# Kernel optimization log

Measured on AMD Instinct MI355X. Metric: run time of the kernel, lower is better.

## Reference

```python
import jax, jax.numpy as jnp
from jax import lax
import numpy as np

B, N_MEL, T_MEL = 256, 80, 800
R = 16                      # n_frames_per_step
RNN = 1024                  # decoder_rnn_dim
ENC = 256                   # token_embedding_size
MEL_DIM = N_MEL * R         # 1280, == RNN + ENC (LSTMCell input size)
IN_DIM = RNN + ENC          # 1280


def setup_inputs() -> dict:
    key = jax.random.key(0)
    ks = jax.random.split(key, 10)
    s = 0.02
    return {
        "context": jax.random.normal(ks[0], (B, ENC), dtype=jnp.float32),
        "target": jax.random.normal(ks[1], (B, N_MEL, T_MEL), dtype=jnp.float32),
        "W_ih": jax.random.normal(ks[2], (4 * RNN, IN_DIM), dtype=jnp.float32) * s,
        "b_ih": jnp.zeros((4 * RNN,), dtype=jnp.float32),
        "W_hh": jax.random.normal(ks[3], (4 * RNN, RNN), dtype=jnp.float32) * s,
        "b_hh": jnp.zeros((4 * RNN,), dtype=jnp.float32),
        "W_proj": jax.random.normal(ks[4], (MEL_DIM, IN_DIM), dtype=jnp.float32) * s,
        "b_proj": jnp.zeros((MEL_DIM,), dtype=jnp.float32),
        "W_gate": jax.random.normal(ks[5], (1, IN_DIM), dtype=jnp.float32) * s,
        "b_gate": jnp.zeros((1,), dtype=jnp.float32),
    }


def _decoder_forward(context, target, W_ih, b_ih, W_hh, b_hh, W_proj, b_proj, W_gate, b_gate):
    b = context.shape[0]
    n_mel, t_mel = target.shape[1], target.shape[2]
    mel_dim = W_proj.shape[0]
    r = mel_dim // n_mel                      # n_frames_per_step
    T = t_mel // r                            # decoder steps
    rnn = W_hh.shape[1]

    # parse_decoder_inputs: [B, n_mel, T_mel] -> [T, B, mel_dim]
    frames = target.transpose(0, 2, 1).reshape(b, T, mel_dim).transpose(1, 0, 2)
    # step 0 uses the all-zeros go frame; step t>=1 uses target frame t (teacher forcing, p=1)
    inputs = frames.at[0].set(0.0)

    h0 = jnp.zeros((b, rnn), dtype=context.dtype)
    c0 = jnp.zeros((b, rnn), dtype=context.dtype)

    def step(carry, x):
        h, c = carry
        gates = x @ W_ih.T + b_ih + h @ W_hh.T + b_hh   # [B, 4*rnn]
        i, f, g, o = jnp.split(gates, 4, axis=-1)        # torch LSTMCell gate order
        c_new = jax.nn.sigmoid(f) * c + jax.nn.sigmoid(i) * jnp.tanh(g)
        h_new = jax.nn.sigmoid(o) * jnp.tanh(c_new)
        # eval mode: dropout on c is identity
        oc = jnp.concatenate([h_new, context], axis=1)   # [B, rnn+enc]
        mel = oc @ W_proj.T + b_proj                     # [B, mel_dim]
        gate = oc @ W_gate.T + b_gate                    # [B, 1]
        return (h_new, c_new), (mel, gate)

    _, (mels, gates) = lax.scan(step, (h0, c0), inputs)
    # mels: [T, B, mel_dim] -> [B, n_mel, T_mel]
    mel_outputs = mels.transpose(1, 0, 2).reshape(b, T * r, n_mel).transpose(0, 2, 1)
    gate_outputs = gates.transpose(1, 0, 2)              # [B, T, 1]
    return mel_outputs, gate_outputs


def reference(context, target, W_ih, b_ih, W_hh, b_hh, W_proj, b_proj, W_gate, b_gate):
    return _decoder_forward(context, target, W_ih, b_ih, W_hh, b_hh,
                            W_proj, b_proj, W_gate, b_gate)
```

## Files before the change

### kernel.cpp

```cpp
#include <hip/hip_runtime.h>
#include <hip/hip_bf16.h>
#include <math.h>

#define BB     256
#define NMEL   80
#define TMEL   800
#define NFR    16
#define TT     50
#define RNN    1024
#define ENC    256
#define INDIM  1280
#define G4     4096
#define MROWS  (TT*BB)

typedef __attribute__((ext_vector_type(8))) short bf16x8;
typedef __attribute__((ext_vector_type(4))) float f32x4;

#define GAS __attribute__((address_space(1)))
#define LAS __attribute__((address_space(3)))

__device__ __forceinline__ unsigned short f2bf(float f) {
    unsigned int u = __float_as_uint(f);
    u += 0x7FFFu + ((u >> 16) & 1u);
    return (unsigned short)(u >> 16);
}
__device__ __forceinline__ float bf2f(unsigned short s) {
    return __uint_as_float(((unsigned int)s) << 16);
}
__device__ __forceinline__ float fsig(float x) {
    return 1.f / (1.f + __expf(-x));
}
__device__ __forceinline__ float ftanh(float x) {
    return 2.f / (1.f + __expf(-2.f * x)) - 1.f;
}


__global__ void k_f32_to_bf16(const float* __restrict__ src,
                              unsigned short* __restrict__ dst, int n4) {
    for (int i = blockIdx.x * blockDim.x + threadIdx.x; i < n4;
         i += gridDim.x * blockDim.x) {
        f32x4 v = *(const f32x4*)(src + (size_t)i * 4);
        unsigned long long p = (unsigned long long)f2bf(v[0]) |
                               ((unsigned long long)f2bf(v[1]) << 16) |
                               ((unsigned long long)f2bf(v[2]) << 32) |
                               ((unsigned long long)f2bf(v[3]) << 48);
        *(unsigned long long*)(dst + (size_t)i * 4) = p;
    }
}

__global__ void k_conv_wph(const float* __restrict__ wproj,
                           unsigned short* __restrict__ dst) {
    const int n4 = INDIM * RNN / 4;
    for (int i = blockIdx.x * blockDim.x + threadIdx.x; i < n4;
         i += gridDim.x * blockDim.x) {
        int mp = i >> 8, kc = (i & 255) * 4;
        int mel = mp >> 4, fr = mp & 15;
        f32x4 v = *(const f32x4*)(wproj + (size_t)(fr * NMEL + mel) * INDIM + kc);
        unsigned long long p = (unsigned long long)f2bf(v[0]) |
                               ((unsigned long long)f2bf(v[1]) << 16) |
                               ((unsigned long long)f2bf(v[2]) << 32) |
                               ((unsigned long long)f2bf(v[3]) << 48);
        *(unsigned long long*)(dst + (size_t)i * 4) = p;
    }
}

__global__ void k_conv_wpc(const float* __restrict__ wproj,
                           unsigned short* __restrict__ dst) {
    const int n4 = INDIM * ENC / 4;
    for (int i = blockIdx.x * blockDim.x + threadIdx.x; i < n4;
         i += gridDim.x * blockDim.x) {
        int mp = i >> 6, kc = (i & 63) * 4;
        int mel = mp >> 4, fr = mp & 15;
        f32x4 v = *(const f32x4*)(wproj + (size_t)(fr * NMEL + mel) * INDIM +
                                  RNN + kc);
        unsigned long long p = (unsigned long long)f2bf(v[0]) |
                               ((unsigned long long)f2bf(v[1]) << 16) |
                               ((unsigned long long)f2bf(v[2]) << 32) |
                               ((unsigned long long)f2bf(v[3]) << 48);
        *(unsigned long long*)(dst + (size_t)i * 4) = p;
    }
}

__global__ __launch_bounds__(128) void k_frames(const float* __restrict__ target,
                                                unsigned short* __restrict__ frames) {
    const int wg = blockIdx.x;
    const int t = wg >> 8, b = wg & 255;
    unsigned short* dst = frames + ((size_t)t * BB + b) * INDIM;
    if (t == 0) {
        for (int i = threadIdx.x; i < INDIM / 8; i += 128)
            *(f32x4*)(dst + i * 8) = (f32x4){0.f, 0.f, 0.f, 0.f};
        return;
    }
    __shared__ float ld[NMEL][17];
    for (int i = threadIdx.x; i < 320; i += 128) {
        const int mel = i >> 2, fq = i & 3;
        f32x4 v = *(const f32x4*)(target + ((size_t)b * NMEL + mel) * TMEL +
                                  t * NFR + fq * 4);
        #pragma unroll
        for (int j = 0; j < 4; ++j) ld[mel][fq * 4 + j] = v[j];
    }
    __syncthreads();
    for (int i = threadIdx.x; i < 160; i += 128) {
        unsigned long long p0 = 0, p1 = 0;
        #pragma unroll
        for (int j = 0; j < 4; ++j) {
            const int k = i * 8 + j;
            p0 |= (unsigned long long)f2bf(ld[k % 80][k / 80]) << (16 * j);
        }
        #pragma unroll
        for (int j = 0; j < 4; ++j) {
            const int k = i * 8 + 4 + j;
            p1 |= (unsigned long long)f2bf(ld[k % 80][k / 80]) << (16 * j);
        }
        *(unsigned long long*)(dst + i * 8) = p0;
        *(unsigned long long*)(dst + i * 8 + 4) = p1;
    }
}

__global__ void k_gatectx(const float* __restrict__ context,
                          const float* __restrict__ wgate,
                          const float* __restrict__ bgate,
                          float* __restrict__ gctx) {
    int b = blockIdx.x * blockDim.x + threadIdx.x;
    if (b >= BB) return;
    float acc = bgate[0];
    const float* cb = context + b * ENC;
    for (int e = 0; e < ENC; ++e) acc += cb[e] * wgate[RNN + e];
    gctx[b] = acc;
}

template<int STRIDE, int KDIM>
__device__ __forceinline__ void gemm_core3(const unsigned short* __restrict__ A,
                                           const unsigned short* __restrict__ Bw,
                                           int mblk, int nblk,
                                           unsigned short* As,
                                           unsigned short* Bs,
                                           f32x4 acc[4][2]) {
    const int tid = threadIdx.x, lane = tid & 63, w = tid >> 6;
    const int lr = lane & 15, q = lane >> 4;
    const int wm = (w >> 2) * 64, wn = (w & 3) * 32;
    const int cc1 = tid, cc2 = tid + 512;
    const int r1 = cc1 >> 3, s1 = ((cc1 & 7) ^ (r1 & 7)) * 8;
    const int r2 = cc2 >> 3, s2 = ((cc2 & 7) ^ (r2 & 7)) * 8;
    const unsigned short* a1p = A + (size_t)(mblk + r1) * STRIDE + s1;
    const unsigned short* a2p = A + (size_t)(mblk + r2) * STRIDE + s2;
    const unsigned short* b1p = Bw + (size_t)(nblk + r1) * STRIDE + s1;
    const unsigned short* b2p = Bw + (size_t)(nblk + r2) * STRIDE + s2;

#define GSTAGE(buf, k0) do {                                                   \
    __builtin_amdgcn_global_load_lds((const GAS unsigned int*)(a1p + (k0)),    \
        (LAS unsigned int*)(As + (buf) * 8192 + w * 512), 16, 0, 0);           \
    __builtin_amdgcn_global_load_lds((const GAS unsigned int*)(a2p + (k0)),    \
        (LAS unsigned int*)(As + (buf) * 8192 + 4096 + w * 512), 16, 0, 0);    \
    __builtin_amdgcn_global_load_lds((const GAS unsigned int*)(b1p + (k0)),    \
        (LAS unsigned int*)(Bs + (buf) * 8192 + w * 512), 16, 0, 0);           \
    __builtin_amdgcn_global_load_lds((const GAS unsigned int*)(b2p + (k0)),    \
        (LAS unsigned int*)(Bs + (buf) * 8192 + 4096 + w * 512), 16, 0, 0); } while (0)

    constexpr int NIT = KDIM / 64;
    GSTAGE(0, 0); GSTAGE(1, 64);
    #pragma unroll 3
    for (int it = 0; it < NIT; ++it) {
        if (it < NIT - 1) asm volatile("s_waitcnt vmcnt(4)" ::: "memory");
        else              asm volatile("s_waitcnt vmcnt(0)" ::: "memory");
        asm volatile("s_waitcnt lgkmcnt(0)" ::: "memory");
        asm volatile("s_barrier" ::: "memory");
        __builtin_amdgcn_sched_barrier(0);
        if (it <= NIT - 3) GSTAGE((it + 2) % 3, (it + 2) * 64);
        const unsigned short* Ab = As + (it % 3) * 8192;
        const unsigned short* Bb = Bs + (it % 3) * 8192;
        #pragma unroll
        for (int ks = 0; ks < 2; ++ks) {
            const int j = (((ks * 4 + q) ^ (lr & 7)) * 8);
            bf16x8 af[4], bv[2];
            #pragma unroll
            for (int mi = 0; mi < 4; ++mi)
                af[mi] = *(const bf16x8*)(Ab + (wm + mi * 16 + lr) * 64 + j);
            #pragma unroll
            for (int ni = 0; ni < 2; ++ni)
                bv[ni] = *(const bf16x8*)(Bb + (wn + ni * 16 + lr) * 64 + j);
            #pragma unroll
            for (int mi = 0; mi < 4; ++mi)
                #pragma unroll
                for (int ni = 0; ni < 2; ++ni)
                    acc[mi][ni] = __builtin_amdgcn_mfma_f32_16x16x32_bf16(
                        af[mi], bv[ni], acc[mi][ni], 0, 0, 0);
        }
    }
#undef GSTAGE
}

__global__ __launch_bounds__(512) void k_gemm_xproj(
    const unsigned short* __restrict__ A,
    const unsigned short* __restrict__ Bw,
    const float* __restrict__ b_ih, const float* __restrict__ b_hh,
    unsigned short* __restrict__ Cout)
{
    __shared__ unsigned short As[3][8192], Bs[3][8192];
    f32x4 acc[4][2] = {};
    const int mblk = blockIdx.y * 128, nblk = blockIdx.x * 128;
    gemm_core3<INDIM, INDIM>(A, Bw, mblk, nblk, &As[0][0], &Bs[0][0], acc);
    const int lane = threadIdx.x & 63, w = threadIdx.x >> 6;
    const int wm = (w >> 2) * 64, wn = (w & 3) * 32;
    const int lr = lane & 15, q = lane >> 4;
    #pragma unroll
    for (int ni = 0; ni < 2; ++ni) {
        const int col = nblk + wn + ni * 16 + lr;
        const float bias = b_ih[col] + b_hh[col];
        #pragma unroll
        for (int mi = 0; mi < 4; ++mi) {
            const int row0 = mblk + wm + mi * 16 + q * 4;
            #pragma unroll
            for (int r = 0; r < 4; ++r)
                Cout[(size_t)(row0 + r) * G4 + col] = f2bf(acc[mi][ni][r] + bias);
        }
    }
}

__global__ __launch_bounds__(512) void k_gemm_mel(
    const unsigned short* __restrict__ A,
    const unsigned short* __restrict__ Bw,
    const float* __restrict__ ctxproj,
    float* __restrict__ out0)
{
    __shared__ unsigned short As[3][8192], Bs[3][8192];
    __shared__ float txp[8][16][20];
    f32x4 acc[4][2] = {};
    const int mblk = blockIdx.y * 128, nblk = blockIdx.x * 128;
    gemm_core3<RNN, RNN>(A, Bw, mblk, nblk, &As[0][0], &Bs[0][0], acc);
    const int lane = threadIdx.x & 63, w = threadIdx.x >> 6;
    const int wm = (w >> 2) * 64, wn = (w & 3) * 32;
    const int lr = lane & 15, q = lane >> 4;
    const int rbase = q * 4;
    const int rowl = lane & 15, fq = lane >> 4;
    #pragma unroll
    for (int mi = 0; mi < 4; ++mi) {
        const int row0 = mblk + wm + mi * 16;
        const int t = row0 >> 8, b0 = row0 & 255;
        #pragma unroll
        for (int ni = 0; ni < 2; ++ni) {
            const int colbase = nblk + wn + ni * 16;
            const int mel = colbase >> 4;
            #pragma unroll
            for (int r = 0; r < 4; ++r)
                txp[w][rbase + r][lr] = acc[mi][ni][r];
            const int bL = b0 + rowl;
            f32x4 v = *(const f32x4*)&txp[w][rowl][fq * 4];
            f32x4 cx = *(const f32x4*)(ctxproj + (size_t)bL * INDIM +
                                       mel * 16 + fq * 4);
            *(f32x4*)(out0 + (size_t)(bL * NMEL + mel) * TMEL +
                      t * NFR + fq * 4) = v + cx;
        }
    }
}

__global__ __launch_bounds__(512) void k_gemm_ctx(
    const unsigned short* __restrict__ A,
    const unsigned short* __restrict__ Bw,
    const float* __restrict__ bproj,
    float* __restrict__ ctxout)
{
    __shared__ unsigned short As[3][8192], Bs[3][8192];
    f32x4 acc[4][2] = {};
    const int mblk = blockIdx.y * 128, nblk = blockIdx.x * 128;
    gemm_core3<ENC, ENC>(A, Bw, mblk, nblk, &As[0][0], &Bs[0][0], acc);
    const int lane = threadIdx.x & 63, w = threadIdx.x >> 6;
    const int wm = (w >> 2) * 64, wn = (w & 3) * 32;
    const int lr = lane & 15, q = lane >> 4;
    #pragma unroll
    for (int ni = 0; ni < 2; ++ni) {
        const int mp = nblk + wn + ni * 16 + lr;
        const int mel = mp >> 4, fr = mp & 15;
        const float bias = bproj[fr * NMEL + mel];
        #pragma unroll
        for (int mi = 0; mi < 4; ++mi) {
            const int b0 = mblk + wm + mi * 16 + q * 4;
            #pragma unroll
            for (int r = 0; r < 4; ++r)
                ctxout[(size_t)(b0 + r) * INDIM + mp] = acc[mi][ni][r] + bias;
        }
    }
}

__global__ __launch_bounds__(512) void k_step(
    const unsigned short* __restrict__ Whh,
    const unsigned short* __restrict__ xproj_t,
    const unsigned short* __restrict__ h_prev,
    unsigned short* __restrict__ h_next,
    float* __restrict__ c)
{
    __shared__ unsigned short Abuf[3][8192];
    __shared__ unsigned short Bbuf[3][8192];
    __shared__ unsigned short xg[4096];
    __shared__ float cld[64][16];
    __shared__ float gates[4][64][17];
    const int tid = threadIdx.x, lane = tid & 63, w = tid >> 6;
    const int g = w & 3, mh = w >> 2;
    const int n0 = blockIdx.x * 16, m0 = blockIdx.y * 64;
    const int lr = lane & 15, q = lane >> 4;

    const int cc1 = tid, cc2 = tid + 512;
    const int r1 = cc1 >> 4, s1g = (cc1 & 15) ^ (r1 & 15);
    const int r2 = cc2 >> 4, s2g = (cc2 & 15) ^ (r2 & 15);
    const unsigned short* a1src = h_prev + (size_t)(m0 + r1) * RNN + s1g * 8;
    const unsigned short* a2src = h_prev + (size_t)(m0 + r2) * RNN + s2g * 8;
    const unsigned short* b1src = Whh +
        (size_t)((r1 >> 4) * RNN + n0 + (r1 & 15)) * RNN + s1g * 8;
    const unsigned short* b2src = Whh +
        (size_t)((r2 >> 4) * RNN + n0 + (r2 & 15)) * RNN + s2g * 8;
    const unsigned short* xsrc = xproj_t +
        (size_t)(m0 + ((tid >> 1) & 63)) * G4 + (tid >> 7) * RNN + n0 +
        (tid & 1) * 8;
    const float* csrc = c + (size_t)(m0 + (tid >> 2)) * RNN + n0 + (tid & 3) * 4;

#define STAGE(buf, k0) do {                                                    \
    __builtin_amdgcn_global_load_lds((const GAS unsigned int*)(a1src + (k0)),  \
        (LAS unsigned int*)&Abuf[buf][w * 512], 16, 0, 0);                     \
    __builtin_amdgcn_global_load_lds((const GAS unsigned int*)(a2src + (k0)),  \
        (LAS unsigned int*)&Abuf[buf][4096 + w * 512], 16, 0, 0);              \
    __builtin_amdgcn_global_load_lds((const GAS unsigned int*)(b1src + (k0)),  \
        (LAS unsigned int*)&Bbuf[buf][w * 512], 16, 0, 0);                     \
    __builtin_amdgcn_global_load_lds((const GAS unsigned int*)(b2src + (k0)),  \
        (LAS unsigned int*)&Bbuf[buf][4096 + w * 512], 16, 0, 0); } while (0)

    if (w < 4)
        __builtin_amdgcn_global_load_lds((const GAS unsigned int*)csrc,
            (LAS unsigned int*)&cld[w * 16][0], 16, 0, 0);
    __builtin_amdgcn_global_load_lds((const GAS unsigned int*)xsrc,
        (LAS unsigned int*)&xg[w * 512], 16, 0, 0);
    STAGE(0, 0); STAGE(1, 128);

    f32x4 acc[2] = {};
    #pragma unroll
    for (int it = 0; it < 8; ++it) {
        if (it <= 6) asm volatile("s_waitcnt vmcnt(4)" ::: "memory");
        else         asm volatile("s_waitcnt vmcnt(0)" ::: "memory");
        asm volatile("s_waitcnt lgkmcnt(0)" ::: "memory");
        asm volatile("s_barrier" ::: "memory");
        __builtin_amdgcn_sched_barrier(0);
        if (it <= 5) STAGE((it + 2) % 3, (it + 2) * 128);
        const unsigned short* Ab = Abuf[it % 3];
        const unsigned short* Bb = Bbuf[it % 3];
        #pragma unroll
        for (int ks = 0; ks < 4; ++ks) {
            const int j = ((ks * 4 + q) ^ lr) * 8;
            bf16x8 a0 = *(const bf16x8*)(Ab + (mh * 32 + lr) * 128 + j);
            bf16x8 a1 = *(const bf16x8*)(Ab + (mh * 32 + 16 + lr) * 128 + j);
            bf16x8 bv = *(const bf16x8*)(Bb + (g * 16 + lr) * 128 + j);
            acc[0] = __builtin_amdgcn_mfma_f32_16x16x32_bf16(a0, bv, acc[0], 0, 0, 0);
            acc[1] = __builtin_amdgcn_mfma_f32_16x16x32_bf16(a1, bv, acc[1], 0, 0, 0);
        }
    }

    #pragma unroll
    for (int mi = 0; mi < 2; ++mi)
        #pragma unroll
        for (int r = 0; r < 4; ++r) {
            const int row = mh * 32 + mi * 16 + q * 4 + r;
            gates[g][row][lr] = acc[mi][r] +
                bf2f(xg[(g * 64 + row) * 16 + lr]);
        }
    __syncthreads();

    #pragma unroll
    for (int q2 = 0; q2 < 2; ++q2) {
        const int e = tid + q2 * 512;
        const int row = e >> 4, col = e & 15;
        const int b = m0 + row, j = n0 + col;
        const float xi = gates[0][row][col];
        const float xf = gates[1][row][col];
        const float xgt = gates[2][row][col];
        const float xo = gates[3][row][col];
        const float si = fsig(xi);
        const float sf = fsig(xf);
        const float so = fsig(xo);
        const float cp = cld[row][col];
        const float cn = sf * cp + si * ftanh(xgt);
        const float hn = so * ftanh(cn);
        c[(size_t)b * RNN + j] = cn;
        h_next[(size_t)b * RNN + j] = f2bf(hn);
    }
#undef STAGE
}

__global__ void k_gate(const unsigned short* __restrict__ h,
                       const float* __restrict__ wgate,
                       const float* __restrict__ gctx,
                       float* __restrict__ out1) {
    const int gw = (blockIdx.x * blockDim.x + threadIdx.x) >> 6;
    const int lane = threadIdx.x & 63;
    if (gw >= MROWS) return;
    const unsigned short* hr = h + (size_t)gw * RNN + lane * 16;
    const float* wr = wgate + lane * 16;
    float acc = 0.f;
    #pragma unroll
    for (int j = 0; j < 16; ++j) acc += bf2f(hr[j]) * wr[j];
    for (int off = 32; off; off >>= 1) acc += __shfl_down(acc, off);
    if (lane == 0) {
        const int t = gw >> 8, b = gw & 255;
        out1[b * TT + t] = acc + gctx[b];
    }
}

static const size_t OFF_WIH   = 0;
static const size_t OFF_WHH   = OFF_WIH   + (size_t)G4 * INDIM * 2;
static const size_t OFF_WPH   = OFF_WHH   + (size_t)G4 * RNN * 2;
static const size_t OFF_WPC   = OFF_WPH   + (size_t)INDIM * RNN * 2;
static const size_t OFF_CTXB  = OFF_WPC   + (size_t)INDIM * ENC * 2;
static const size_t OFF_FRM   = OFF_CTXB  + (size_t)BB * ENC * 2;
static const size_t OFF_XPROJ = OFF_FRM   + (size_t)MROWS * INDIM * 2;
static const size_t OFF_HALL  = OFF_XPROJ + (size_t)MROWS * G4 * 2;
static const size_t OFF_C     = OFF_HALL  + (size_t)(TT + 1) * BB * RNN * 2;
static const size_t OFF_CTX   = OFF_C     + (size_t)BB * RNN * 4;
static const size_t OFF_GCTX  = OFF_CTX   + (size_t)BB * INDIM * 4;

extern "C" void kernel_launch(void* const* d_in, const int* in_sizes, int n_in,
                              void* d_out, int out_size, void* d_ws, size_t ws_size,
                              hipStream_t stream) {
    const float* context = (const float*)d_in[0];
    const float* target  = (const float*)d_in[1];
    const float* W_ih    = (const float*)d_in[2];
    const float* b_ih    = (const float*)d_in[3];
    const float* W_hh    = (const float*)d_in[4];
    const float* b_hh    = (const float*)d_in[5];
    const float* W_proj  = (const float*)d_in[6];
    const float* b_proj  = (const float*)d_in[7];
    const float* W_gate  = (const float*)d_in[8];
    const float* b_gate  = (const float*)d_in[9];
    float* out = (float*)d_out;
    char* ws = (char*)d_ws;

    unsigned short* wih_bf  = (unsigned short*)(ws + OFF_WIH);
    unsigned short* whh_bf  = (unsigned short*)(ws + OFF_WHH);
    unsigned short* wph_bf  = (unsigned short*)(ws + OFF_WPH);
    unsigned short* wpc_bf  = (unsigned short*)(ws + OFF_WPC);
    unsigned short* ctx_bf  = (unsigned short*)(ws + OFF_CTXB);
    unsigned short* frames  = (unsigned short*)(ws + OFF_FRM);
    unsigned short* xproj   = (unsigned short*)(ws + OFF_XPROJ);
    unsigned short* h_all   = (unsigned short*)(ws + OFF_HALL);
    float*          c_buf   = (float*)(ws + OFF_C);
    float*          ctxproj = (float*)(ws + OFF_CTX);
    float*          gctx    = (float*)(ws + OFF_GCTX);

    hipMemsetAsync(h_all, 0, (size_t)BB * RNN * 2, stream);
    hipMemsetAsync(c_buf, 0, (size_t)BB * RNN * 4, stream);

    k_f32_to_bf16<<<2048, 256, 0, stream>>>(W_ih, wih_bf, G4 * INDIM / 4);
    k_f32_to_bf16<<<2048, 256, 0, stream>>>(W_hh, whh_bf, G4 * RNN / 4);
    k_conv_wph<<<2048, 256, 0, stream>>>(W_proj, wph_bf);
    k_conv_wpc<<<320, 256, 0, stream>>>(W_proj, wpc_bf);
    k_f32_to_bf16<<<64, 256, 0, stream>>>(context, ctx_bf, BB * ENC / 4);
    k_frames<<<MROWS, 128, 0, stream>>>(target, frames);
    k_gatectx<<<1, 256, 0, stream>>>(context, W_gate, b_gate, gctx);

    k_gemm_ctx<<<dim3(INDIM / 128, BB / 128), 512, 0, stream>>>(
        ctx_bf, wpc_bf, b_proj, ctxproj);

    k_gemm_xproj<<<dim3(G4 / 128, MROWS / 128), 512, 0, stream>>>(
        frames, wih_bf, b_ih, b_hh, xproj);

    for (int t = 0; t < TT; ++t) {
        k_step<<<dim3(64, 4), 512, 0, stream>>>(
            whh_bf, xproj + (size_t)t * BB * G4,
            h_all + (size_t)t * BB * RNN,
            h_all + (size_t)(t + 1) * BB * RNN, c_buf);
    }

    k_gemm_mel<<<dim3(INDIM / 128, MROWS / 128), 512, 0, stream>>>(
        h_all + (size_t)BB * RNN, wph_bf, ctxproj, out);
    k_gate<<<MROWS / 4, 256, 0, stream>>>(h_all + (size_t)BB * RNN, W_gate,
                                          gctx, out + (size_t)BB * NMEL * TMEL);
}
```

Measured before the change: 729.7 us.

## Use double-buffered GEMM pipeline and smaller K-tiles in recurrent step kernel

The shared GEMM core changes from a triple-buffered, two-ahead prefetch to a double-buffered scheme. It issues the next stage before waiting and adds a trailing barrier after compute. This lowers LDS usage per block, which may raise occupancy, but costs an extra barrier per K iteration. The per-step LSTM recurrent kernel now uses 64-wide K tiles with 16 iterations instead of 128-wide with 8, halving its LDS staging buffers. In exchange it runs more loop iterations and barriers inside the latency-critical sequential step.

```diff
diff --git a/kernel.cpp b/kernel.cpp
--- a/kernel.cpp
+++ b/kernel.cpp
@@ -130,7 +130,7 @@
 }
 
 template<int STRIDE, int KDIM>
-__device__ __forceinline__ void gemm_core3(const unsigned short* __restrict__ A,
+__device__ __forceinline__ void gemm_core2(const unsigned short* __restrict__ A,
                                            const unsigned short* __restrict__ Bw,
                                            int mblk, int nblk,
                                            unsigned short* As,
@@ -158,17 +158,19 @@
         (LAS unsigned int*)(Bs + (buf) * 8192 + 4096 + w * 512), 16, 0, 0); } while (0)
 
     constexpr int NIT = KDIM / 64;
-    GSTAGE(0, 0); GSTAGE(1, 64);
-    #pragma unroll 3
+    GSTAGE(0, 0);
+    #pragma unroll 4
     for (int it = 0; it < NIT; ++it) {
-        if (it < NIT - 1) asm volatile("s_waitcnt vmcnt(4)" ::: "memory");
-        else              asm volatile("s_waitcnt vmcnt(0)" ::: "memory");
-        asm volatile("s_waitcnt lgkmcnt(0)" ::: "memory");
+        if (it < NIT - 1) {
+            GSTAGE((it + 1) & 1, (it + 1) * 64);
+            asm volatile("s_waitcnt vmcnt(4)" ::: "memory");
+        } else {
+            asm volatile("s_waitcnt vmcnt(0)" ::: "memory");
+        }
         asm volatile("s_barrier" ::: "memory");
         __builtin_amdgcn_sched_barrier(0);
-        if (it <= NIT - 3) GSTAGE((it + 2) % 3, (it + 2) * 64);
-        const unsigned short* Ab = As + (it % 3) * 8192;
-        const unsigned short* Bb = Bs + (it % 3) * 8192;
+        const unsigned short* Ab = As + (it & 1) * 8192;
+        const unsigned short* Bb = Bs + (it & 1) * 8192;
         #pragma unroll
         for (int ks = 0; ks < 2; ++ks) {
             const int j = (((ks * 4 + q) ^ (lr & 7)) * 8);
@@ -186,6 +188,9 @@
                     acc[mi][ni] = __builtin_amdgcn_mfma_f32_16x16x32_bf16(
                         af[mi], bv[ni], acc[mi][ni], 0, 0, 0);
         }
+        asm volatile("s_waitcnt lgkmcnt(0)" ::: "memory");
+        __builtin_amdgcn_sched_barrier(0);
+        asm volatile("s_barrier" ::: "memory");
     }
 #undef GSTAGE
 }
@@ -196,10 +201,10 @@
     const float* __restrict__ b_ih, const float* __restrict__ b_hh,
     unsigned short* __restrict__ Cout)
 {
-    __shared__ unsigned short As[3][8192], Bs[3][8192];
+    __shared__ unsigned short As[2][8192], Bs[2][8192];
     f32x4 acc[4][2] = {};
     const int mblk = blockIdx.y * 128, nblk = blockIdx.x * 128;
-    gemm_core3<INDIM, INDIM>(A, Bw, mblk, nblk, &As[0][0], &Bs[0][0], acc);
+    gemm_core2<INDIM, INDIM>(A, Bw, mblk, nblk, &As[0][0], &Bs[0][0], acc);
     const int lane = threadIdx.x & 63, w = threadIdx.x >> 6;
     const int wm = (w >> 2) * 64, wn = (w & 3) * 32;
     const int lr = lane & 15, q = lane >> 4;
@@ -223,11 +228,11 @@
     const float* __restrict__ ctxproj,
     float* __restrict__ out0)
 {
-    __shared__ unsigned short As[3][8192], Bs[3][8192];
+    __shared__ unsigned short As[2][8192], Bs[2][8192];
     __shared__ float txp[8][16][20];
     f32x4 acc[4][2] = {};
     const int mblk = blockIdx.y * 128, nblk = blockIdx.x * 128;
-    gemm_core3<RNN, RNN>(A, Bw, mblk, nblk, &As[0][0], &Bs[0][0], acc);
+    gemm_core2<RNN, RNN>(A, Bw, mblk, nblk, &As[0][0], &Bs[0][0], acc);
     const int lane = threadIdx.x & 63, w = threadIdx.x >> 6;
     const int wm = (w >> 2) * 64, wn = (w & 3) * 32;
     const int lr = lane & 15, q = lane >> 4;
@@ -260,10 +265,10 @@
     const float* __restrict__ bproj,
     float* __restrict__ ctxout)
 {
-    __shared__ unsigned short As[3][8192], Bs[3][8192];
+    __shared__ unsigned short As[2][8192], Bs[2][8192];
     f32x4 acc[4][2] = {};
     const int mblk = blockIdx.y * 128, nblk = blockIdx.x * 128;
-    gemm_core3<ENC, ENC>(A, Bw, mblk, nblk, &As[0][0], &Bs[0][0], acc);
+    gemm_core2<ENC, ENC>(A, Bw, mblk, nblk, &As[0][0], &Bs[0][0], acc);
     const int lane = threadIdx.x & 63, w = threadIdx.x >> 6;
     const int wm = (w >> 2) * 64, wn = (w & 3) * 32;
     const int lr = lane & 15, q = lane >> 4;
@@ -289,8 +294,8 @@
     unsigned short* __restrict__ h_next,
     float* __restrict__ c)
 {
-    __shared__ unsigned short Abuf[3][8192];
-    __shared__ unsigned short Bbuf[3][8192];
+    __shared__ unsigned short Abuf[3][4096];
+    __shared__ unsigned short Bbuf[3][4096];
     __shared__ unsigned short xg[4096];
     __shared__ float cld[64][16];
     __shared__ float gates[4][64][17];
@@ -299,54 +304,46 @@
     const int n0 = blockIdx.x * 16, m0 = blockIdx.y * 64;
     const int lr = lane & 15, q = lane >> 4;
 
-    const int cc1 = tid, cc2 = tid + 512;
-    const int r1 = cc1 >> 4, s1g = (cc1 & 15) ^ (r1 & 15);
-    const int r2 = cc2 >> 4, s2g = (cc2 & 15) ^ (r2 & 15);
-    const unsigned short* a1src = h_prev + (size_t)(m0 + r1) * RNN + s1g * 8;
-    const unsigned short* a2src = h_prev + (size_t)(m0 + r2) * RNN + s2g * 8;
-    const unsigned short* b1src = Whh +
-        (size_t)((r1 >> 4) * RNN + n0 + (r1 & 15)) * RNN + s1g * 8;
-    const unsigned short* b2src = Whh +
-        (size_t)((r2 >> 4) * RNN + n0 + (r2 & 15)) * RNN + s2g * 8;
+    const int rowc = tid >> 3, sc = ((tid & 7) ^ (rowc & 7)) * 8;
+    const unsigned short* asrc = h_prev + (size_t)(m0 + rowc) * RNN + sc;
+    const unsigned short* bsrc = Whh +
+        (size_t)((rowc >> 4) * RNN + n0 + (rowc & 15)) * RNN + sc;
     const unsigned short* xsrc = xproj_t +
         (size_t)(m0 + ((tid >> 1) & 63)) * G4 + (tid >> 7) * RNN + n0 +
         (tid & 1) * 8;
     const float* csrc = c + (size_t)(m0 + (tid >> 2)) * RNN + n0 + (tid & 3) * 4;
 
 #define STAGE(buf, k0) do {                                                    \
-    __builtin_amdgcn_global_load_lds((const GAS unsigned int*)(a1src + (k0)),  \
+    __builtin_amdgcn_global_load_lds((const GAS unsigned int*)(asrc + (k0)),   \
         (LAS unsigned int*)&Abuf[buf][w * 512], 16, 0, 0);                     \
-    __builtin_amdgcn_global_load_lds((const GAS unsigned int*)(a2src + (k0)),  \
-        (LAS unsigned int*)&Abuf[buf][4096 + w * 512], 16, 0, 0);              \
-    __builtin_amdgcn_global_load_lds((const GAS unsigned int*)(b1src + (k0)),  \
-        (LAS unsigned int*)&Bbuf[buf][w * 512], 16, 0, 0);                     \
-    __builtin_amdgcn_global_load_lds((const GAS unsigned int*)(b2src + (k0)),  \
-        (LAS unsigned int*)&Bbuf[buf][4096 + w * 512], 16, 0, 0); } while (0)
+    __builtin_amdgcn_global_load_lds((const GAS unsigned int*)(bsrc + (k0)),   \
+        (LAS unsigned int*)&Bbuf[buf][w * 512], 16, 0, 0); } while (0)
 
     if (w < 4)
         __builtin_amdgcn_global_load_lds((const GAS unsigned int*)csrc,
             (LAS unsigned int*)&cld[w * 16][0], 16, 0, 0);
     __builtin_amdgcn_global_load_lds((const GAS unsigned int*)xsrc,
         (LAS unsigned int*)&xg[w * 512], 16, 0, 0);
-    STAGE(0, 0); STAGE(1, 128);
+    STAGE(0, 0); STAGE(1, 64); STAGE(2, 128);
 
     f32x4 acc[2] = {};
     #pragma unroll
-    for (int it = 0; it < 8; ++it) {
-        if (it <= 6) asm volatile("s_waitcnt vmcnt(4)" ::: "memory");
-        else         asm volatile("s_waitcnt vmcnt(0)" ::: "memory");
+    for (int it = 0; it < 16; ++it) {
+        if (it <= 13)      asm volatile("s_waitcnt vmcnt(4)" ::: "memory");
+        else if (it == 14) asm volatile("s_waitcnt vmcnt(2)" ::: "memory");
+        else               asm volatile("s_waitcnt vmcnt(0)" ::: "memory");
         asm volatile("s_waitcnt lgkmcnt(0)" ::: "memory");
         asm volatile("s_barrier" ::: "memory");
         __builtin_amdgcn_sched_barrier(0);
-        if (it <= 5) STAGE((it + 2) % 3, (it + 2) * 128);
+        if (it <= 13) STAGE((it + 2) % 3, (it + 2) * 64);
         const unsigned short* Ab = Abuf[it % 3];
         const unsigned short* Bb = Bbuf[it % 3];
         #pragma unroll
-        for (int ks = 0; ks < 4; ++ks) {
-            const int j = ((ks * 4 + q) ^ lr) * 8;
-            bf16x8 a0 = *(const bf16x8*)(Ab + (mh * 32 + lr) * 128 + j);
-            bf16x8 a1 = *(const bf16x8*)(Ab + (mh * 32 + 16 + lr) * 128 + j);
-            bf16x8 bv = *(const bf16x8*)(Bb + (g * 16 + lr) * 128 + j);
+        for (int ks = 0; ks < 2; ++ks) {
+            const int j = (((ks * 4 + q) ^ (lr & 7)) * 8);
+            bf16x8 a0 = *(const bf16x8*)(Ab + (mh * 32 + lr) * 64 + j);
+            bf16x8 a1 = *(const bf16x8*)(Ab + (mh * 32 + 16 + lr) * 64 + j);
+            bf16x8 bv = *(const bf16x8*)(Bb + (g * 16 + lr) * 64 + j);
             acc[0] = __builtin_amdgcn_mfma_f32_16x16x32_bf16(a0, bv, acc[0], 0, 0, 0);
             acc[1] = __builtin_amdgcn_mfma_f32_16x16x32_bf16(a1, bv, acc[1], 0, 0, 0);
         }
```

New measurement: 801.5 us. 1.1x slower.

## Restructure batched GEMMs to 4 waves with 64x64 warp tiles and fragment-major LDS

Applied to the files above, without the earlier changes.

The shared GEMM core moves from 8 waves with 64x32 warp tiles and a BK=64 XOR-swizzled LDS stage to 4 waves with 64x64 warp tiles and a BK=32 stage. The stage is stored in MFMA fragment order, so each lane reads its 16-byte operand at lane*8 with no swizzle. The aim is more MFMA work per LDS fragment load and a smaller LDS footprint, which could allow more blocks per CU. The cost is twice as many k-iterations and barriers per tile, and more accumulator registers per thread. Only the pre- and post-recurrence GEMMs change; the 50 sequential step kernels are untouched.

```diff
diff --git a/kernel.cpp b/kernel.cpp
--- a/kernel.cpp
+++ b/kernel.cpp
@@ -130,81 +130,76 @@
 }
 
 template<int STRIDE, int KDIM>
-__device__ __forceinline__ void gemm_core3(const unsigned short* __restrict__ A,
+__device__ __forceinline__ void gemm_core4(const unsigned short* __restrict__ A,
                                            const unsigned short* __restrict__ Bw,
                                            int mblk, int nblk,
                                            unsigned short* As,
                                            unsigned short* Bs,
-                                           f32x4 acc[4][2]) {
+                                           f32x4 acc[4][4]) {
     const int tid = threadIdx.x, lane = tid & 63, w = tid >> 6;
-    const int lr = lane & 15, q = lane >> 4;
-    const int wm = (w >> 2) * 64, wn = (w & 3) * 32;
-    const int cc1 = tid, cc2 = tid + 512;
-    const int r1 = cc1 >> 3, s1 = ((cc1 & 7) ^ (r1 & 7)) * 8;
-    const int r2 = cc2 >> 3, s2 = ((cc2 & 7) ^ (r2 & 7)) * 8;
-    const unsigned short* a1p = A + (size_t)(mblk + r1) * STRIDE + s1;
-    const unsigned short* a2p = A + (size_t)(mblk + r2) * STRIDE + s2;
-    const unsigned short* b1p = Bw + (size_t)(nblk + r1) * STRIDE + s1;
-    const unsigned short* b2p = Bw + (size_t)(nblk + r2) * STRIDE + s2;
+    const int wm = (w >> 1) * 64, wn = (w & 1) * 64;
+    const int c1 = tid, c2 = tid + 256;
+    const int r1 = (c1 >> 6) * 16 + (c1 & 15), k1 = ((c1 >> 4) & 3) * 8;
+    const int r2 = (c2 >> 6) * 16 + (c2 & 15), k2 = ((c2 >> 4) & 3) * 8;
+    const unsigned short* a1p = A + (size_t)(mblk + r1) * STRIDE + k1;
+    const unsigned short* a2p = A + (size_t)(mblk + r2) * STRIDE + k2;
+    const unsigned short* b1p = Bw + (size_t)(nblk + r1) * STRIDE + k1;
+    const unsigned short* b2p = Bw + (size_t)(nblk + r2) * STRIDE + k2;
 
 #define GSTAGE(buf, k0) do {                                                   \
     __builtin_amdgcn_global_load_lds((const GAS unsigned int*)(a1p + (k0)),    \
-        (LAS unsigned int*)(As + (buf) * 8192 + w * 512), 16, 0, 0);           \
+        (LAS unsigned int*)(As + (buf) * 4096 + w * 512), 16, 0, 0);           \
     __builtin_amdgcn_global_load_lds((const GAS unsigned int*)(a2p + (k0)),    \
-        (LAS unsigned int*)(As + (buf) * 8192 + 4096 + w * 512), 16, 0, 0);    \
+        (LAS unsigned int*)(As + (buf) * 4096 + 2048 + w * 512), 16, 0, 0);    \
     __builtin_amdgcn_global_load_lds((const GAS unsigned int*)(b1p + (k0)),    \
-        (LAS unsigned int*)(Bs + (buf) * 8192 + w * 512), 16, 0, 0);           \
+        (LAS unsigned int*)(Bs + (buf) * 4096 + w * 512), 16, 0, 0);           \
     __builtin_amdgcn_global_load_lds((const GAS unsigned int*)(b2p + (k0)),    \
-        (LAS unsigned int*)(Bs + (buf) * 8192 + 4096 + w * 512), 16, 0, 0); } while (0)
-
-    constexpr int NIT = KDIM / 64;
-    GSTAGE(0, 0); GSTAGE(1, 64);
-    #pragma unroll 3
+        (LAS unsigned int*)(Bs + (buf) * 4096 + 2048 + w * 512), 16, 0, 0); } while (0)
+
+    constexpr int NIT = KDIM / 32;
+    GSTAGE(0, 0); GSTAGE(1, 32);
+    #pragma unroll 4
     for (int it = 0; it < NIT; ++it) {
         if (it < NIT - 1) asm volatile("s_waitcnt vmcnt(4)" ::: "memory");
         else              asm volatile("s_waitcnt vmcnt(0)" ::: "memory");
         asm volatile("s_waitcnt lgkmcnt(0)" ::: "memory");
         asm volatile("s_barrier" ::: "memory");
         __builtin_amdgcn_sched_barrier(0);
-        if (it <= NIT - 3) GSTAGE((it + 2) % 3, (it + 2) * 64);
-        const unsigned short* Ab = As + (it % 3) * 8192;
-        const unsigned short* Bb = Bs + (it % 3) * 8192;
-        #pragma unroll
-        for (int ks = 0; ks < 2; ++ks) {
-            const int j = (((ks * 4 + q) ^ (lr & 7)) * 8);
-            bf16x8 af[4], bv[2];
+        if (it <= NIT - 3) GSTAGE((it + 2) % 3, (it + 2) * 32);
+        const unsigned short* Ab = As + (it % 3) * 4096;
+        const unsigned short* Bb = Bs + (it % 3) * 4096;
+        bf16x8 af[4], bv[4];
+        #pragma unroll
+        for (int mi = 0; mi < 4; ++mi)
+            af[mi] = *(const bf16x8*)(Ab + ((wm >> 4) + mi) * 512 + lane * 8);
+        #pragma unroll
+        for (int ni = 0; ni < 4; ++ni)
+            bv[ni] = *(const bf16x8*)(Bb + ((wn >> 4) + ni) * 512 + lane * 8);
+        #pragma unroll
+        for (int mi = 0; mi < 4; ++mi)
             #pragma unroll
-            for (int mi = 0; mi < 4; ++mi)
-                af[mi] = *(const bf16x8*)(Ab + (wm + mi * 16 + lr) * 64 + j);
-            #pragma unroll
-            for (int ni = 0; ni < 2; ++ni)
-                bv[ni] = *(const bf16x8*)(Bb + (wn + ni * 16 + lr) * 64 + j);
-            #pragma unroll
-            for (int mi = 0; mi < 4; ++mi)
-                #pragma unroll
-                for (int ni = 0; ni < 2; ++ni)
-                    acc[mi][ni] = __builtin_amdgcn_mfma_f32_16x16x32_bf16(
-                        af[mi], bv[ni], acc[mi][ni], 0, 0, 0);
-        }
+            for (int ni = 0; ni < 4; ++ni)
+                acc[mi][ni] = __builtin_amdgcn_mfma_f32_16x16x32_bf16(
+                    af[mi], bv[ni], acc[mi][ni], 0, 0, 0);
     }
 #undef GSTAGE
 }
 
-__global__ __launch_bounds__(512) void k_gemm_xproj(
+__global__ __launch_bounds__(256) void k_gemm_xproj(
     const unsigned short* __restrict__ A,
     const unsigned short* __restrict__ Bw,
     const float* __restrict__ b_ih, const float* __restrict__ b_hh,
     unsigned short* __restrict__ Cout)
 {
-    __shared__ unsigned short As[3][8192], Bs[3][8192];
-    f32x4 acc[4][2] = {};
+    __shared__ unsigned short As[3][4096], Bs[3][4096];
+    f32x4 acc[4][4] = {};
     const int mblk = blockIdx.y * 128, nblk = blockIdx.x * 128;
-    gemm_core3<INDIM, INDIM>(A, Bw, mblk, nblk, &As[0][0], &Bs[0][0], acc);
+    gemm_core4<INDIM, INDIM>(A, Bw, mblk, nblk, &As[0][0], &Bs[0][0], acc);
     const int lane = threadIdx.x & 63, w = threadIdx.x >> 6;
-    const int wm = (w >> 2) * 64, wn = (w & 3) * 32;
+    const int wm = (w >> 1) * 64, wn = (w & 1) * 64;
     const int lr = lane & 15, q = lane >> 4;
     #pragma unroll
-    for (int ni = 0; ni < 2; ++ni) {
+    for (int ni = 0; ni < 4; ++ni) {
         const int col = nblk + wn + ni * 16 + lr;
         const float bias = b_ih[col] + b_hh[col];
         #pragma unroll
@@ -217,19 +212,19 @@
     }
 }
 
-__global__ __launch_bounds__(512) void k_gemm_mel(
+__global__ __launch_bounds__(256) void k_gemm_mel(
     const unsigned short* __restrict__ A,
     const unsigned short* __restrict__ Bw,
     const float* __restrict__ ctxproj,
     float* __restrict__ out0)
 {
-    __shared__ unsigned short As[3][8192], Bs[3][8192];
-    __shared__ float txp[8][16][20];
-    f32x4 acc[4][2] = {};
+    __shared__ unsigned short As[3][4096], Bs[3][4096];
+    __shared__ float txp[4][16][20];
+    f32x4 acc[4][4] = {};
     const int mblk = blockIdx.y * 128, nblk = blockIdx.x * 128;
-    gemm_core3<RNN, RNN>(A, Bw, mblk, nblk, &As[0][0], &Bs[0][0], acc);
+    gemm_core4<RNN, RNN>(A, Bw, mblk, nblk, &As[0][0], &Bs[0][0], acc);
     const int lane = threadIdx.x & 63, w = threadIdx.x >> 6;
-    const int wm = (w >> 2) * 64, wn = (w & 3) * 32;
+    const int wm = (w >> 1) * 64, wn = (w & 1) * 64;
     const int lr = lane & 15, q = lane >> 4;
     const int rbase = q * 4;
     const int rowl = lane & 15, fq = lane >> 4;
@@ -238,7 +233,7 @@
         const int row0 = mblk + wm + mi * 16;
         const int t = row0 >> 8, b0 = row0 & 255;
         #pragma unroll
-        for (int ni = 0; ni < 2; ++ni) {
+        for (int ni = 0; ni < 4; ++ni) {
             const int colbase = nblk + wn + ni * 16;
             const int mel = colbase >> 4;
             #pragma unroll
@@ -254,21 +249,21 @@
     }
 }
 
-__global__ __launch_bounds__(512) void k_gemm_ctx(
+__global__ __launch_bounds__(256) void k_gemm_ctx(
     const unsigned short* __restrict__ A,
     const unsigned short* __restrict__ Bw,
     const float* __restrict__ bproj,
     float* __restrict__ ctxout)
 {
-    __shared__ unsigned short As[3][8192], Bs[3][8192];
-    f32x4 acc[4][2] = {};
+    __shared__ unsigned short As[3][4096], Bs[3][4096];
+    f32x4 acc[4][4] = {};
     const int mblk = blockIdx.y * 128, nblk = blockIdx.x * 128;
-    gemm_core3<ENC, ENC>(A, Bw, mblk, nblk, &As[0][0], &Bs[0][0], acc);
+    gemm_core4<ENC, ENC>(A, Bw, mblk, nblk, &As[0][0], &Bs[0][0], acc);
     const int lane = threadIdx.x & 63, w = threadIdx.x >> 6;
-    const int wm = (w >> 2) * 64, wn = (w & 3) * 32;
+    const int wm = (w >> 1) * 64, wn = (w & 1) * 64;
     const int lr = lane & 15, q = lane >> 4;
     #pragma unroll
-    for (int ni = 0; ni < 2; ++ni) {
+    for (int ni = 0; ni < 4; ++ni) {
         const int mp = nblk + wn + ni * 16 + lr;
         const int mel = mp >> 4, fr = mp & 15;
         const float bias = bproj[fr * NMEL + mel];
@@ -453,10 +448,10 @@
     k_frames<<<MROWS, 128, 0, stream>>>(target, frames);
     k_gatectx<<<1, 256, 0, stream>>>(context, W_gate, b_gate, gctx);
 
-    k_gemm_ctx<<<dim3(INDIM / 128, BB / 128), 512, 0, stream>>>(
+    k_gemm_ctx<<<dim3(INDIM / 128, BB / 128), 256, 0, stream>>>(
         ctx_bf, wpc_bf, b_proj, ctxproj);
 
-    k_gemm_xproj<<<dim3(G4 / 128, MROWS / 128), 512, 0, stream>>>(
+    k_gemm_xproj<<<dim3(G4 / 128, MROWS / 128), 256, 0, stream>>>(
         frames, wih_bf, b_ih, b_hh, xproj);
 
     for (int t = 0; t < TT; ++t) {
@@ -466,7 +461,7 @@
             h_all + (size_t)(t + 1) * BB * RNN, c_buf);
     }
 
-    k_gemm_mel<<<dim3(INDIM / 128, MROWS / 128), 512, 0, stream>>>(
+    k_gemm_mel<<<dim3(INDIM / 128, MROWS / 128), 256, 0, stream>>>(
         h_all + (size_t)BB * RNN, wph_bf, ctxproj, out);
     k_gate<<<MROWS / 4, 256, 0, stream>>>(h_all + (size_t)BB * RNN, W_gate,
                                           gctx, out + (size_t)BB * NMEL * TMEL);
```

Result: slower. 861.4 us (+18.0%).
